# Performance work log

Hardware: AMD Instinct MI355X
Metric: run time of the kernel (lower is better)

## Reference

```python
import jax, jax.numpy as jnp
import numpy as np
import math

B, H, W, CIN = 4, 64, 64, 256
G, C, K = 8, 32, 9
MAX_SCALE = 6.0


def setup_inputs() -> dict:
    key = jax.random.key(0)
    ks = jax.random.split(key, 10)
    s = 0.02
    x = jax.random.normal(ks[0], (B, H, W, CIN), dtype=jnp.float32)
    # linear params stored as [in, out]
    v_w = jax.random.normal(ks[1], (CIN, G * C), dtype=jnp.float32) * s
    v_b = jax.random.normal(ks[2], (G * C,), dtype=jnp.float32) * s
    qd_w = jax.random.normal(ks[3], (CIN, G * K * 2), dtype=jnp.float32) * s
    qd_b = jax.random.normal(ks[4], (G * K * 2,), dtype=jnp.float32) * s
    qs_w = jax.random.normal(ks[5], (CIN, G * K), dtype=jnp.float32) * s  # no bias
    qw_w = jax.random.normal(ks[6], (CIN, G * K), dtype=jnp.float32) * s
    qw_b = jax.random.normal(ks[7], (G * K,), dtype=jnp.float32) * s
    out_w = jax.random.normal(ks[8], (G * C, CIN), dtype=jnp.float32) * s
    out_b = jax.random.normal(ks[9], (CIN,), dtype=jnp.float32) * s
    # deformables_prior: 3x3 grid in [-1,1], meshgrid indexing='xy', stacked (x,y)
    n = int(math.isqrt(K))
    d = np.linspace(-1.0, 1.0, n, dtype=np.float32)
    gx, gy = np.meshgrid(d, d, indexing='xy')
    prior = jnp.asarray(np.stack([gx, gy], axis=-1).reshape(1, 1, 1, 1, K, 2))
    # deformables_scale: per-group inverse-sigmoid of (i+1)/G - 1e-4
    sc = np.array([(i + 1) / G - 1e-4 for i in range(G)], dtype=np.float32)
    dscale = jnp.asarray(np.log(sc / (1.0 - sc)).reshape(1, 1, 1, G, 1, 1))
    return dict(x=x, v_w=v_w, v_b=v_b, qd_w=qd_w, qd_b=qd_b, qs_w=qs_w,
                qw_w=qw_w, qw_b=qw_b, out_w=out_w, out_b=out_b,
                prior=prior, dscale=dscale)


def _dcn_sample(v, deform, weights):
    # v: [B,H,W,G,C]; deform: [B,H,W,G,K,2] pixel offsets (x,y); weights: [B,H,W,G,K]
    b_, h_, w_, g_, c_ = v.shape
    ww = jnp.arange(w_, dtype=v.dtype)[None, None, :, None, None]
    hh = jnp.arange(h_, dtype=v.dtype)[None, :, None, None, None]
    px = ww + deform[..., 0]  # [B,H,W,G,K]
    py = hh + deform[..., 1]
    x0 = jnp.floor(px); y0 = jnp.floor(py)
    wx1 = px - x0; wx0 = 1.0 - wx1
    wy1 = py - y0; wy0 = 1.0 - wy1
    bidx = jnp.arange(b_)[:, None, None, None, None]
    gidx = jnp.arange(g_)[None, None, None, :, None]

    def gather(yi, xi):
        valid = ((yi >= 0) & (yi < h_) & (xi >= 0) & (xi < w_)).astype(v.dtype)
        yc = jnp.clip(yi, 0, h_ - 1).astype(jnp.int32)
        xc = jnp.clip(xi, 0, w_ - 1).astype(jnp.int32)
        return v[bidx, yc, xc, gidx] * valid[..., None]  # [B,H,W,G,K,C]

    samp = (gather(y0, x0) * (wy0 * wx0)[..., None]
            + gather(y0, x0 + 1) * (wy0 * wx1)[..., None]
            + gather(y0 + 1, x0) * (wy1 * wx0)[..., None]
            + gather(y0 + 1, x0 + 1) * (wy1 * wx1)[..., None])
    # weighted sum over kernels -> [B,H,W,G,C]
    return jnp.einsum('bhwgkc,bhwgk->bhwgc', samp, weights)


def reference(x, v_w, v_b, qd_w, qd_b, qs_w, qw_w, qw_b, out_w, out_b, prior, dscale):
    b_, h_, w_, _ = x.shape
    v = (x @ v_w + v_b).reshape(b_, h_, w_, G, C)
    deform = (x @ qd_w + qd_b).reshape(b_, h_, w_, G, K, 2)
    scale = (x @ qs_w).reshape(b_, h_, w_, G, K, 1) + dscale
    deform = (deform + prior) * jax.nn.sigmoid(scale) * MAX_SCALE
    weights = (x @ qw_w + qw_b).reshape(b_, h_, w_, G, K)
    out = _dcn_sample(v, deform, weights)  # [B,H,W,G,C]
    out = out.reshape(b_, h_, w_, G * C)
    return out @ out_w + out_b
```

## Files before the change

kernel.cpp:

```cpp
#include <hip/hip_runtime.h>

#define NPIX 16384

typedef __attribute__((ext_vector_type(8))) short short8;
typedef __attribute__((ext_vector_type(4))) float f32x4;

__device__ __forceinline__ unsigned short f2bf(float f) {
    unsigned u = __float_as_uint(f);
    unsigned r = (u + 0x7fffu + ((u >> 16) & 1u)) >> 16;
    return (unsigned short)r;
}

#define GLOAD16(SRC, DST) \
    __builtin_amdgcn_global_load_lds( \
        (const __attribute__((address_space(1))) unsigned*)(SRC), \
        (__attribute__((address_space(3))) unsigned*)(DST), 16, 0, 0)

__device__ __forceinline__ float wsrc(int k, int n,
    const float* v_w, const float* qd_w, const float* qs_w,
    const float* qw_w, const float* out_w)
{
    if (n < 256) return v_w[k * 256 + n];
    n -= 256;
    if (n < 144) return qd_w[k * 144 + n];
    n -= 144;
    if (n < 72)  return qs_w[k * 72 + n];
    n -= 72;
    if (n < 72)  return qw_w[k * 72 + n];
    n -= 72;
    if (n < 32)  return 0.f;
    return out_w[k * 256 + (n - 32)];
}

__global__ __launch_bounds__(256) void prep_wt(
    const float* __restrict__ v_w, const float* __restrict__ qd_w,
    const float* __restrict__ qs_w, const float* __restrict__ qw_w,
    const float* __restrict__ out_w, const float* __restrict__ qd_b,
    const float* __restrict__ qw_b,
    unsigned short* __restrict__ Wt, float* __restrict__ biasD)
{
    const int tid = threadIdx.x;
    if (blockIdx.x == 52) {
        for (int i = tid; i < 320; i += 256) {
            float bv = 0.f;
            if (i < 144)                  bv = qd_b[i];
            else if (i >= 216 && i < 288) bv = qw_b[i - 216];
            biasD[i] = bv;
        }
        return;
    }
    __shared__ float t[64][65];
    const int tn = blockIdx.x % 13;
    const int tk = blockIdx.x / 13;
    #pragma unroll
    for (int i = 0; i < 16; ++i) {
        const int idx = tid + i * 256;
        const int r = idx >> 6;
        const int c = idx & 63;
        t[r][c] = wsrc(tk * 64 + r, tn * 64 + c, v_w, qd_w, qs_w, qw_w, out_w);
    }
    __syncthreads();
    #pragma unroll
    for (int i = 0; i < 8; ++i) {
        const int idx = tid + i * 256;
        const int rn = idx >> 5;
        const int cc = idx & 31;
        const unsigned pk = (unsigned)f2bf(t[cc * 2][rn])
                          | ((unsigned)f2bf(t[cc * 2 + 1][rn]) << 16);
        ((unsigned*)(Wt + (size_t)(tn * 64 + rn) * 256 + tk * 64))[cc] = pk;
    }
}

__global__ __launch_bounds__(256) void gemm_proj(
    const float* __restrict__ x, const unsigned short* __restrict__ Wt,
    const float* __restrict__ v_b, const float* __restrict__ biasD,
    unsigned short* __restrict__ v_bf, float* __restrict__ proj)
{
    __shared__ unsigned short As[64 * 256];
    __shared__ unsigned short Bs[64 * 256];

    const int tid  = threadIdx.x;
    const int wid  = tid >> 6;
    const int lane = tid & 63;
    const int row0 = blockIdx.x * 64;
    const int j    = blockIdx.y;

    const unsigned short* Bb = Wt + (size_t)(j * 64) * 256;
    const int rl = lane >> 5;
    const int gl = lane & 31;
    #pragma unroll
    for (int it = 0; it < 8; ++it) {
        const int rr  = wid * 16 + it * 2 + rl;
        const int gsw = gl ^ (rr & 7);
        GLOAD16(Bb + rr * 256 + gsw * 8, &Bs[(wid * 16 + it * 2) * 256]);
    }

    const float* Ab = x + (size_t)row0 * 256;
    #pragma unroll
    for (int it = 0; it < 8; ++it) {
        const int idx = tid + it * 256;
        const int r   = idx >> 5;
        const int gg  = idx & 31;
        const float4 u0 = *(const float4*)(Ab + r * 256 + gg * 8);
        const float4 u1 = *(const float4*)(Ab + r * 256 + gg * 8 + 4);
        uint4 pk;
        pk.x = f2bf(u0.x) | ((unsigned)f2bf(u0.y) << 16);
        pk.y = f2bf(u0.z) | ((unsigned)f2bf(u0.w) << 16);
        pk.z = f2bf(u1.x) | ((unsigned)f2bf(u1.y) << 16);
        pk.w = f2bf(u1.z) | ((unsigned)f2bf(u1.w) << 16);
        *(uint4*)&As[r * 256 + (gg ^ (r & 7)) * 8] = pk;
    }
    asm volatile("s_waitcnt vmcnt(0)" ::: "memory");
    __syncthreads();

    f32x4 acc00 = {0,0,0,0}, acc01 = {0,0,0,0};
    f32x4 acc10 = {0,0,0,0}, acc11 = {0,0,0,0};

    const int wr = (wid >> 1) * 32;
    const int wc = (wid & 1) * 32;
    const int fr = lane & 15;
    const int fg = lane >> 4;

    const int ra0 = wr + fr, ra1 = ra0 + 16;
    const int rb0 = wc + fr, rb1 = rb0 + 16;
    const int sa  = ra0 & 7;
    const int sb  = rb0 & 7;

    #pragma unroll
    for (int t = 0; t < 8; ++t) {
        const int gran = t * 4 + fg;
        short8 a0 = *(const short8*)&As[ra0 * 256 + (gran ^ sa) * 8];
        short8 a1 = *(const short8*)&As[ra1 * 256 + (gran ^ sa) * 8];
        short8 b0 = *(const short8*)&Bs[rb0 * 256 + (gran ^ sb) * 8];
        short8 b1 = *(const short8*)&Bs[rb1 * 256 + (gran ^ sb) * 8];
        acc00 = __builtin_amdgcn_mfma_f32_16x16x32_bf16(a0, b0, acc00, 0, 0, 0);
        acc01 = __builtin_amdgcn_mfma_f32_16x16x32_bf16(a0, b1, acc01, 0, 0, 0);
        acc10 = __builtin_amdgcn_mfma_f32_16x16x32_bf16(a1, b0, acc10, 0, 0, 0);
        acc11 = __builtin_amdgcn_mfma_f32_16x16x32_bf16(a1, b1, acc11, 0, 0, 0);
    }

    if (j < 4) {
        const int colA = j * 64 + wc + fr;
        const int colB = colA + 16;
        const float biasA = v_b[colA];
        const float biasB = v_b[colB];
        #pragma unroll
        for (int jj = 0; jj < 4; ++jj) {
            const int r0a = row0 + wr + fg * 4 + jj;
            const int r1a = r0a + 16;
            v_bf[(size_t)r0a * 256 + colA] = f2bf(acc00[jj] + biasA);
            v_bf[(size_t)r0a * 256 + colB] = f2bf(acc01[jj] + biasB);
            v_bf[(size_t)r1a * 256 + colA] = f2bf(acc10[jj] + biasA);
            v_bf[(size_t)r1a * 256 + colB] = f2bf(acc11[jj] + biasB);
        }
    } else {
        const int colA = (j - 4) * 64 + wc + fr;
        const int colB = colA + 16;
        const float biasA = biasD[colA];
        const float biasB = biasD[colB];
        #pragma unroll
        for (int jj = 0; jj < 4; ++jj) {
            const int r0a = row0 + wr + fg * 4 + jj;
            const int r1a = r0a + 16;
            proj[(size_t)r0a * 320 + colA] = acc00[jj] + biasA;
            proj[(size_t)r0a * 320 + colB] = acc01[jj] + biasB;
            proj[(size_t)r1a * 320 + colA] = acc10[jj] + biasA;
            proj[(size_t)r1a * 320 + colB] = acc11[jj] + biasB;
        }
    }
}

__global__ __launch_bounds__(256) void gemm_out(
    const unsigned short* __restrict__ A, const unsigned short* __restrict__ WtO,
    const float* __restrict__ bias, float* __restrict__ Y)
{
    __shared__ unsigned short As[64 * 256];
    __shared__ unsigned short Bs[64 * 256];

    const int tid  = threadIdx.x;
    const int wid  = tid >> 6;
    const int lane = tid & 63;
    const int row0 = blockIdx.x * 64;
    const int col0 = blockIdx.y * 64;

    const unsigned short* Ab = A   + (size_t)row0 * 256;
    const unsigned short* Bb = WtO + (size_t)col0 * 256;
    const int rl = lane >> 5;
    const int gl = lane & 31;

    #pragma unroll
    for (int it = 0; it < 8; ++it) {
        const int r   = wid * 16 + it * 2 + rl;
        const int gsw = gl ^ (r & 7);
        GLOAD16(Ab + r * 256 + gsw * 8, &As[(wid * 16 + it * 2) * 256]);
        GLOAD16(Bb + r * 256 + gsw * 8, &Bs[(wid * 16 + it * 2) * 256]);
    }
    asm volatile("s_waitcnt vmcnt(0)" ::: "memory");
    __syncthreads();

    f32x4 acc00 = {0,0,0,0}, acc01 = {0,0,0,0};
    f32x4 acc10 = {0,0,0,0}, acc11 = {0,0,0,0};

    const int wr = (wid >> 1) * 32;
    const int wc = (wid & 1) * 32;
    const int fr = lane & 15;
    const int fg = lane >> 4;

    const int ra0 = wr + fr, ra1 = ra0 + 16;
    const int rb0 = wc + fr, rb1 = rb0 + 16;
    const int sa  = ra0 & 7;
    const int sb  = rb0 & 7;

    #pragma unroll
    for (int t = 0; t < 8; ++t) {
        const int gran = t * 4 + fg;
        short8 a0 = *(const short8*)&As[ra0 * 256 + (gran ^ sa) * 8];
        short8 a1 = *(const short8*)&As[ra1 * 256 + (gran ^ sa) * 8];
        short8 b0 = *(const short8*)&Bs[rb0 * 256 + (gran ^ sb) * 8];
        short8 b1 = *(const short8*)&Bs[rb1 * 256 + (gran ^ sb) * 8];
        acc00 = __builtin_amdgcn_mfma_f32_16x16x32_bf16(a0, b0, acc00, 0, 0, 0);
        acc01 = __builtin_amdgcn_mfma_f32_16x16x32_bf16(a0, b1, acc01, 0, 0, 0);
        acc10 = __builtin_amdgcn_mfma_f32_16x16x32_bf16(a1, b0, acc10, 0, 0, 0);
        acc11 = __builtin_amdgcn_mfma_f32_16x16x32_bf16(a1, b1, acc11, 0, 0, 0);
    }

    const int colA = col0 + wc + fr;
    const int colB = colA + 16;
    const float biasA = bias[colA];
    const float biasB = bias[colB];
    #pragma unroll
    for (int jj = 0; jj < 4; ++jj) {
        const int r0a = row0 + wr + fg * 4 + jj;
        const int r1a = r0a + 16;
        Y[(size_t)r0a * 256 + colA] = acc00[jj] + biasA;
        Y[(size_t)r0a * 256 + colB] = acc01[jj] + biasB;
        Y[(size_t)r1a * 256 + colA] = acc10[jj] + biasA;
        Y[(size_t)r1a * 256 + colB] = acc11[jj] + biasB;
    }
}

__global__ __launch_bounds__(256) void dcn_sample3(
    const unsigned short* __restrict__ vbuf,
    const float* __restrict__ proj,
    const float* __restrict__ prior,
    const float* __restrict__ dscale,
    unsigned short* __restrict__ mid)
{
    __shared__ float projs[8 * 320];
    __shared__ int   offs[576 * 4];
    __shared__ float wts [576 * 4];

    const int tid  = threadIdx.x;
    const int pix0 = blockIdx.x * 8;

    for (int i = tid; i < 640; i += 256) {
        const int p = i / 80, c = i - p * 80;
        *(float4*)&projs[p * 320 + c * 4] =
            *(const float4*)&proj[(size_t)(pix0 + p) * 320 + c * 4];
    }
    __syncthreads();

    for (int it = tid; it < 576; it += 256) {
        const int p   = it / 72;
        const int rem = it - p * 72;
        const int g   = rem / 9;
        const int k   = rem - g * 9;
        const int pix = pix0 + p;
        const int b   = pix >> 12;
        const int hw  = pix & 4095;
        const int h   = hw >> 6, w = hw & 63;

        const float* row = &projs[p * 320];
        const float qdx = row[g * 18 + k * 2 + 0];
        const float qdy = row[g * 18 + k * 2 + 1];
        const float s   = row[144 + g * 9 + k] + dscale[g];
        const float wt  = row[216 + g * 9 + k];
        const float sig6 = 6.0f / (1.0f + __expf(-s));
        const float px = (float)w + (qdx + prior[k * 2 + 0]) * sig6;
        const float py = (float)h + (qdy + prior[k * 2 + 1]) * sig6;

        const float x0f = floorf(px), y0f = floorf(py);
        const int ix = (int)x0f, iy = (int)y0f;
        const float wx1 = px - x0f, wx0 = 1.f - wx1;
        const float wy1 = py - y0f, wy0 = 1.f - wy1;
        const int base_b = b << 12;

        #pragma unroll
        for (int tp = 0; tp < 4; ++tp) {
            const int yy = iy + (tp >> 1), xx = ix + (tp & 1);
            const bool valid = (yy >= 0) & (yy < 64) & (xx >= 0) & (xx < 64);
            const int yc = min(max(yy, 0), 63), xc = min(max(xx, 0), 63);
            const float wgt = wt * ((tp >> 1) ? wy1 : wy0) * ((tp & 1) ? wx1 : wx0);
            offs[it * 4 + tp] = ((base_b + yc * 64 + xc) << 8) + g * 32;
            wts [it * 4 + tp] = valid ? wgt : 0.f;
        }
    }
    __syncthreads();

    const int p  = tid >> 5;
    const int g  = (tid >> 2) & 7;
    const int q  = tid & 3;
    const int c0 = q * 8;
    const int item0 = p * 72 + g * 9;

    float a0=0.f,a1=0.f,a2=0.f,a3=0.f,a4=0.f,a5=0.f,a6=0.f,a7=0.f;
    #pragma unroll
    for (int k = 0; k < 9; ++k) {
        const int it4 = (item0 + k) * 4;
        const int4   o4 = *(const int4*)&offs[it4];
        const float4 w4 = *(const float4*)&wts[it4];
        #pragma unroll
        for (int tp = 0; tp < 4; ++tp) {
            const int   off = (tp == 0) ? o4.x : (tp == 1) ? o4.y : (tp == 2) ? o4.z : o4.w;
            const float wgt = (tp == 0) ? w4.x : (tp == 1) ? w4.y : (tp == 2) ? w4.z : w4.w;
            const uint4 r = *(const uint4*)(vbuf + off + c0);
            a0 = fmaf(wgt, __uint_as_float(r.x << 16),          a0);
            a1 = fmaf(wgt, __uint_as_float(r.x & 0xffff0000u), a1);
            a2 = fmaf(wgt, __uint_as_float(r.y << 16),          a2);
            a3 = fmaf(wgt, __uint_as_float(r.y & 0xffff0000u), a3);
            a4 = fmaf(wgt, __uint_as_float(r.z << 16),          a4);
            a5 = fmaf(wgt, __uint_as_float(r.z & 0xffff0000u), a5);
            a6 = fmaf(wgt, __uint_as_float(r.w << 16),          a6);
            a7 = fmaf(wgt, __uint_as_float(r.w & 0xffff0000u), a7);
        }
    }

    const int pix = pix0 + p;
    unsigned short* mp = mid + (size_t)pix * 256 + g * 32 + c0;
    uint4 o;
    o.x = f2bf(a0) | ((unsigned)f2bf(a1) << 16);
    o.y = f2bf(a2) | ((unsigned)f2bf(a3) << 16);
    o.z = f2bf(a4) | ((unsigned)f2bf(a5) << 16);
    o.w = f2bf(a6) | ((unsigned)f2bf(a7) << 16);
    *(uint4*)mp = o;
}

extern "C" void kernel_launch(void* const* d_in, const int* in_sizes, int n_in,
                              void* d_out, int out_size, void* d_ws, size_t ws_size,
                              hipStream_t stream)
{
    (void)in_sizes; (void)n_in; (void)out_size; (void)ws_size;

    const float* x      = (const float*)d_in[0];
    const float* v_w    = (const float*)d_in[1];
    const float* v_b    = (const float*)d_in[2];
    const float* qd_w   = (const float*)d_in[3];
    const float* qd_b   = (const float*)d_in[4];
    const float* qs_w   = (const float*)d_in[5];
    const float* qw_w   = (const float*)d_in[6];
    const float* qw_b   = (const float*)d_in[7];
    const float* out_w  = (const float*)d_in[8];
    const float* out_b  = (const float*)d_in[9];
    const float* prior  = (const float*)d_in[10];
    const float* dscale = (const float*)d_in[11];
    float* out = (float*)d_out;

    char* ws = (char*)d_ws;
    unsigned short* v_bf  = (unsigned short*)(ws);
    float*          proj  = (float*)(ws + 8388608);
    unsigned short* mid   = (unsigned short*)(ws + 29360128);
    unsigned short* Wt    = (unsigned short*)(ws + 37748736);
    float*          biasD = (float*)(ws + 38175744);

    prep_wt<<<dim3(53), dim3(256), 0, stream>>>(v_w, qd_w, qs_w, qw_w, out_w,
                                                qd_b, qw_b, Wt, biasD);

    gemm_proj<<<dim3(256, 9), dim3(256), 0, stream>>>(x, Wt, v_b, biasD, v_bf, proj);

    dcn_sample3<<<dim3(NPIX / 8), dim3(256), 0, stream>>>(v_bf, proj, prior, dscale, mid);

    gemm_out<<<dim3(256, 4), dim3(256), 0, stream>>>(mid, Wt + 576 * 256, out_b, out);
}
```

Measured before the change: 65.65 us.

## Pre-convert x to bf16, store v group-planar, and remap sampling blocks

x is now converted to bf16 once in a merged prep kernel, so the projection GEMM, which has a 9-wide column grid, loads A through async global-to-LDS copies instead of re-reading and re-converting fp32 x in every column block. The v tensor is written in a [B,G,H,W,C] planar layout so each group's samples come from a compact plane. The sampling blocks are remapped so that concurrently scheduled blocks cover spread-out pixel regions, with the aim of better cache locality. In exchange the prep kernel gains an extra full pass over x and an 8 MB bf16 buffer, and the v stores become more scattered.

```diff
diff --git a/kernel.cpp b/kernel.cpp
--- a/kernel.cpp
+++ b/kernel.cpp
@@ -32,15 +32,31 @@
     return out_w[k * 256 + (n - 32)];
 }
 
-__global__ __launch_bounds__(256) void prep_wt(
+__global__ __launch_bounds__(256) void prep_all(
+    const float* __restrict__ x, unsigned short* __restrict__ xb,
     const float* __restrict__ v_w, const float* __restrict__ qd_w,
     const float* __restrict__ qs_w, const float* __restrict__ qw_w,
     const float* __restrict__ out_w, const float* __restrict__ qd_b,
     const float* __restrict__ qw_b,
     unsigned short* __restrict__ Wt, float* __restrict__ biasD)
 {
+    __shared__ float t[64][65];
+    const int bid = blockIdx.x;
     const int tid = threadIdx.x;
-    if (blockIdx.x == 52) {
+
+    if (bid < 2048) {
+        const size_t i = (size_t)bid * 256 + tid;
+        const float4 v0 = *(const float4*)(x + i * 8);
+        const float4 v1 = *(const float4*)(x + i * 8 + 4);
+        uint4 pk;
+        pk.x = f2bf(v0.x) | ((unsigned)f2bf(v0.y) << 16);
+        pk.y = f2bf(v0.z) | ((unsigned)f2bf(v0.w) << 16);
+        pk.z = f2bf(v1.x) | ((unsigned)f2bf(v1.y) << 16);
+        pk.w = f2bf(v1.z) | ((unsigned)f2bf(v1.w) << 16);
+        *(uint4*)(xb + i * 8) = pk;
+        return;
+    }
+    if (bid == 2100) {
         for (int i = tid; i < 320; i += 256) {
             float bv = 0.f;
             if (i < 144)                  bv = qd_b[i];
@@ -49,9 +65,9 @@
         }
         return;
     }
-    __shared__ float t[64][65];
-    const int tn = blockIdx.x % 13;
-    const int tk = blockIdx.x / 13;
+    const int tile = bid - 2048;
+    const int tn = tile % 13;
+    const int tk = tile / 13;
     #pragma unroll
     for (int i = 0; i < 16; ++i) {
         const int idx = tid + i * 256;
@@ -72,7 +88,7 @@
 }
 
 __global__ __launch_bounds__(256) void gemm_proj(
-    const float* __restrict__ x, const unsigned short* __restrict__ Wt,
+    const unsigned short* __restrict__ A, const unsigned short* __restrict__ Wt,
     const float* __restrict__ v_b, const float* __restrict__ biasD,
     unsigned short* __restrict__ v_bf, float* __restrict__ proj)
 {
@@ -85,30 +101,17 @@
     const int row0 = blockIdx.x * 64;
     const int j    = blockIdx.y;
 
+    const unsigned short* Ab = A  + (size_t)row0 * 256;
     const unsigned short* Bb = Wt + (size_t)(j * 64) * 256;
     const int rl = lane >> 5;
     const int gl = lane & 31;
+
     #pragma unroll
     for (int it = 0; it < 8; ++it) {
-        const int rr  = wid * 16 + it * 2 + rl;
-        const int gsw = gl ^ (rr & 7);
-        GLOAD16(Bb + rr * 256 + gsw * 8, &Bs[(wid * 16 + it * 2) * 256]);
-    }
-
-    const float* Ab = x + (size_t)row0 * 256;
-    #pragma unroll
-    for (int it = 0; it < 8; ++it) {
-        const int idx = tid + it * 256;
-        const int r   = idx >> 5;
-        const int gg  = idx & 31;
-        const float4 u0 = *(const float4*)(Ab + r * 256 + gg * 8);
-        const float4 u1 = *(const float4*)(Ab + r * 256 + gg * 8 + 4);
-        uint4 pk;
-        pk.x = f2bf(u0.x) | ((unsigned)f2bf(u0.y) << 16);
-        pk.y = f2bf(u0.z) | ((unsigned)f2bf(u0.w) << 16);
-        pk.z = f2bf(u1.x) | ((unsigned)f2bf(u1.y) << 16);
-        pk.w = f2bf(u1.z) | ((unsigned)f2bf(u1.w) << 16);
-        *(uint4*)&As[r * 256 + (gg ^ (r & 7)) * 8] = pk;
+        const int r   = wid * 16 + it * 2 + rl;
+        const int gsw = gl ^ (r & 7);
+        GLOAD16(Ab + r * 256 + gsw * 8, &As[(wid * 16 + it * 2) * 256]);
+        GLOAD16(Bb + r * 256 + gsw * 8, &Bs[(wid * 16 + it * 2) * 256]);
     }
     asm volatile("s_waitcnt vmcnt(0)" ::: "memory");
     __syncthreads();
@@ -142,16 +145,20 @@
     if (j < 4) {
         const int colA = j * 64 + wc + fr;
         const int colB = colA + 16;
+        const int gA = colA >> 5, cA = colA & 31;
+        const int gB = colB >> 5, cB = colB & 31;
         const float biasA = v_b[colA];
         const float biasB = v_b[colB];
         #pragma unroll
         for (int jj = 0; jj < 4; ++jj) {
             const int r0a = row0 + wr + fg * 4 + jj;
             const int r1a = r0a + 16;
-            v_bf[(size_t)r0a * 256 + colA] = f2bf(acc00[jj] + biasA);
-            v_bf[(size_t)r0a * 256 + colB] = f2bf(acc01[jj] + biasB);
-            v_bf[(size_t)r1a * 256 + colA] = f2bf(acc10[jj] + biasA);
-            v_bf[(size_t)r1a * 256 + colB] = f2bf(acc11[jj] + biasB);
+            const int b0i = r0a >> 12;
+            const int hw0 = r0a & 4095, hw1 = r1a & 4095;
+            v_bf[((size_t)(b0i * 8 + gA) * 4096 + hw0) * 32 + cA] = f2bf(acc00[jj] + biasA);
+            v_bf[((size_t)(b0i * 8 + gB) * 4096 + hw0) * 32 + cB] = f2bf(acc01[jj] + biasB);
+            v_bf[((size_t)(b0i * 8 + gA) * 4096 + hw1) * 32 + cA] = f2bf(acc10[jj] + biasA);
+            v_bf[((size_t)(b0i * 8 + gB) * 4096 + hw1) * 32 + cB] = f2bf(acc11[jj] + biasB);
         }
     } else {
         const int colA = (j - 4) * 64 + wc + fr;
@@ -239,7 +246,7 @@
     }
 }
 
-__global__ __launch_bounds__(256) void dcn_sample3(
+__global__ __launch_bounds__(256) void dcn_sample4(
     const unsigned short* __restrict__ vbuf,
     const float* __restrict__ proj,
     const float* __restrict__ prior,
@@ -250,8 +257,10 @@
     __shared__ int   offs[576 * 4];
     __shared__ float wts [576 * 4];
 
-    const int tid  = threadIdx.x;
-    const int pix0 = blockIdx.x * 8;
+    const int tid = threadIdx.x;
+    const int bid  = blockIdx.x;
+    const int wg   = (bid & 7) * 256 + (bid >> 3);
+    const int pix0 = wg * 8;
 
     for (int i = tid; i < 640; i += 256) {
         const int p = i / 80, c = i - p * 80;
@@ -283,7 +292,7 @@
         const int ix = (int)x0f, iy = (int)y0f;
         const float wx1 = px - x0f, wx0 = 1.f - wx1;
         const float wy1 = py - y0f, wy0 = 1.f - wy1;
-        const int base_b = b << 12;
+        const int plane = (b * 8 + g) << 12;
 
         #pragma unroll
         for (int tp = 0; tp < 4; ++tp) {
@@ -291,7 +300,7 @@
             const bool valid = (yy >= 0) & (yy < 64) & (xx >= 0) & (xx < 64);
             const int yc = min(max(yy, 0), 63), xc = min(max(xx, 0), 63);
             const float wgt = wt * ((tp >> 1) ? wy1 : wy0) * ((tp & 1) ? wx1 : wx0);
-            offs[it * 4 + tp] = ((base_b + yc * 64 + xc) << 8) + g * 32;
+            offs[it * 4 + tp] = (plane + yc * 64 + xc) * 32;
             wts [it * 4 + tp] = valid ? wgt : 0.f;
         }
     }
@@ -356,18 +365,19 @@
     float* out = (float*)d_out;
 
     char* ws = (char*)d_ws;
-    unsigned short* v_bf  = (unsigned short*)(ws);
-    float*          proj  = (float*)(ws + 8388608);
-    unsigned short* mid   = (unsigned short*)(ws + 29360128);
-    unsigned short* Wt    = (unsigned short*)(ws + 37748736);
-    float*          biasD = (float*)(ws + 38175744);
-
-    prep_wt<<<dim3(53), dim3(256), 0, stream>>>(v_w, qd_w, qs_w, qw_w, out_w,
-                                                qd_b, qw_b, Wt, biasD);
-
-    gemm_proj<<<dim3(256, 9), dim3(256), 0, stream>>>(x, Wt, v_b, biasD, v_bf, proj);
-
-    dcn_sample3<<<dim3(NPIX / 8), dim3(256), 0, stream>>>(v_bf, proj, prior, dscale, mid);
+    unsigned short* xb    = (unsigned short*)(ws);
+    unsigned short* v_bf  = (unsigned short*)(ws + 8388608);
+    float*          proj  = (float*)(ws + 16777216);
+    unsigned short* mid   = (unsigned short*)(ws + 37748736);
+    unsigned short* Wt    = (unsigned short*)(ws + 46137344);
+    float*          biasD = (float*)(ws + 46563328);
+
+    prep_all<<<dim3(2101), dim3(256), 0, stream>>>(x, xb, v_w, qd_w, qs_w, qw_w,
+                                                   out_w, qd_b, qw_b, Wt, biasD);
+
+    gemm_proj<<<dim3(256, 9), dim3(256), 0, stream>>>(xb, Wt, v_b, biasD, v_bf, proj);
+
+    dcn_sample4<<<dim3(NPIX / 8), dim3(256), 0, stream>>>(v_bf, proj, prior, dscale, mid);
 
     gemm_out<<<dim3(256, 4), dim3(256), 0, stream>>>(mid, Wt + 576 * 256, out_b, out);
 }
```

After: 58.25 us. 11.3% less time.
